# Performance work log

Hardware: AMD Instinct MI355X
Metric: run time of the kernel (lower is better)

## Reference

```python
import jax, jax.numpy as jnp
import numpy as np

B, F, T, D, O = 8192, 512, 64, 6, 128
N_INTERNAL = 2 ** D - 1  # 63
N_LEAVES = 2 ** D        # 64


def smooth_step(t):
    tc = jnp.clip(t, -0.5, 0.5)
    return -2.0 * tc ** 3 + 1.5 * tc + 0.5


def setup_inputs() -> dict:
    key = jax.random.key(0)
    k1, k2, k3, k4 = jax.random.split(key, 4)
    x = jax.random.normal(k1, (B, F), dtype=jnp.float32)
    # Stacked per-node Linear weights in BFS (heap) order: node i -> row i.
    W_nodes = jax.random.normal(k2, (N_INTERNAL, F, T), dtype=jnp.float32) * (1.0 / np.sqrt(F))
    b_nodes = jax.random.normal(k3, (N_INTERNAL, T), dtype=jnp.float32) * 0.01
    # Per-leaf mixing weight [out_features, num_trees], leaves in BFS order.
    W_leaf = jax.random.normal(k4, (N_LEAVES, O, T), dtype=jnp.float32)
    return {"x": x, "W_nodes": W_nodes, "b_nodes": b_nodes, "W_leaf": W_leaf}


def reference(x, W_nodes, b_nodes, W_leaf):
    n_internal = W_nodes.shape[0]
    depth = int(np.log2(n_internal + 1))
    # All internal-node gates in one stacked GEMM: [B, n_internal, T]
    s = smooth_step(jnp.einsum('bf,nft->bnt', x, W_nodes) + b_nodes[None, :, :])
    b, _, t = s.shape
    prob = jnp.ones((b, 1, t), dtype=s.dtype)  # root prob
    start = 0
    for lvl in range(depth):
        width = 2 ** lvl
        s_l = s[:, start:start + width]  # [B, width, T], nodes at this level
        start += width
        # node local j -> children local 2j (left, prob*s) and 2j+1 (right, prob*(1-s))
        prob = jnp.stack([prob * s_l, prob * (1.0 - s_l)], axis=2).reshape(b, 2 * width, t)
    # prob: [B, n_leaves, T]; mix per-leaf, per-tree weights -> [B, O]
    out = jnp.einsum('blt,lot->bo', prob, W_leaf)
    return out
```

## Files before the change

kernel.cpp:

```cpp
#include <hip/hip_runtime.h>
#include <hip/hip_fp16.h>

#define BATCH 8192
#define FDIM  512
#define NTREE 64
#define NODES 63
#define ODIM  128
#define NJP   4096
#define K2    4096
#define TPG   8

typedef _Float16 f16;
typedef _Float16 f16x2 __attribute__((ext_vector_type(2)));
typedef _Float16 f16x4 __attribute__((ext_vector_type(4)));
typedef _Float16 f16x8 __attribute__((ext_vector_type(8)));
typedef float    f32x4 __attribute__((ext_vector_type(4)));

#define XH_OFF   0
#define XH_SZ    ((size_t)BATCH*FDIM*2)
#define WNH_OFF  (XH_OFF + XH_SZ)
#define WNH_SZ   ((size_t)NJP*FDIM*2)
#define WLT_OFF  (WNH_OFF + WNH_SZ)
#define WLT_SZ   ((size_t)ODIM*K2*2)
#define WS_NEEDED (WLT_OFF + WLT_SZ)

__device__ __forceinline__ float smooth_step_f(float t) {
    float tc = fminf(fmaxf(t, -0.5f), 0.5f);
    return fmaf(tc, fmaf(-2.0f * tc, tc, 1.5f), 0.5f);
}

__device__ __forceinline__ int sw_off(int row, int g) {
    return ((row >> 3) * 512) + (((row & 7) * 8 + (g ^ (row & 7))) * 8);
}

__global__ __launch_bounds__(256)
void prep_kernel(const float* __restrict__ x, const float* __restrict__ wn,
                 const float* __restrict__ wl,
                 f16* __restrict__ xf, f16* __restrict__ wnf, f16* __restrict__ wlf,
                 float* __restrict__ out)
{
    const int bid = blockIdx.x, tid = threadIdx.x;
    if (bid >= 832) {
        size_t i = ((size_t)(bid - 832) * 256 + tid) * 4;
        f32x4 z = {};
        *(f32x4*)(out + i) = z;
        return;
    }
    if (bid < 512) {
        const int bx = bid >> 3, k0 = bid & 7;
        f16* dst = xf + ((size_t)bx * 8192 + (size_t)k0 * 1024) * 8;
        #pragma unroll
        for (int c = 0; c < 4; ++c) {
            int fid  = c * 256 + tid;
            int lane = fid & 63, ks = (fid >> 6) & 1, rg = (fid >> 7) & 7;
            int row  = bx * 128 + rg * 16 + (lane & 15);
            int k    = k0 * 64 + (ks * 4 + (lane >> 4)) * 8;
            const float* s = x + (size_t)row * FDIM + k;
            float4 a = *(const float4*)s, b = *(const float4*)(s + 4);
            f16x8 v = { (f16)a.x, (f16)a.y, (f16)a.z, (f16)a.w,
                        (f16)b.x, (f16)b.y, (f16)b.z, (f16)b.w };
            *(f16x8*)(dst + (size_t)fid * 8) = v;
        }
    } else if (bid < 768) {
        const int id = bid - 512;
        const int t0 = (id >> 4) * 4;
        const int n  = tid & 63;
        const int k8 = (id & 15) * 4 + (tid >> 6);
        float4 q[8];
        if (n != NODES) {
            #pragma unroll
            for (int e = 0; e < 8; ++e)
                q[e] = *(const float4*)(wn + ((size_t)n * FDIM + k8 * 8 + e) * NTREE + t0);
        }
        #pragma unroll
        for (int j = 0; j < 4; ++j) {
            int t  = t0 + j;
            int tp = t >> 1;
            int cg = (t & 1) * 4 + (n >> 4);
            size_t chunk = (size_t)tp * 8192 + (size_t)(k8 >> 3) * 1024 + cg * 128
                         + ((k8 >> 2) & 1) * 64 + (k8 & 3) * 16 + (n & 15);
            f16x8 v;
            if (n == NODES) {
                #pragma unroll
                for (int e = 0; e < 8; ++e) v[e] = (f16)0.0f;
            } else {
                const float* qf = (const float*)q;
                #pragma unroll
                for (int e = 0; e < 8; ++e) v[e] = (f16)qf[e * 4 + j];
            }
            *(f16x8*)(wnf + chunk * 8) = v;
        }
    } else {
        const int id = bid - 768;
        const int t0 = (id >> 2) * 4;
        const int o  = tid & 127;
        const int l8 = (id & 3) * 2 + (tid >> 7);
        float4 q[8];
        #pragma unroll
        for (int e = 0; e < 8; ++e)
            q[e] = *(const float4*)(wl + ((size_t)(l8 * 8 + e) * ODIM + o) * NTREE + t0);
        #pragma unroll
        for (int j = 0; j < 4; ++j) {
            int t  = t0 + j;
            int tp = t >> 1, h = t & 1;
            size_t chunk = (size_t)tp * 2048 + (size_t)h * 1024 + (o >> 4) * 128
                         + (l8 >> 2) * 64 + (l8 & 3) * 16 + (o & 15);
            const float* qf = (const float*)q;
            f16x8 v;
            #pragma unroll
            for (int e = 0; e < 8; ++e) v[e] = (f16)qf[e * 4 + j];
            *(f16x8*)(wlf + chunk * 8) = v;
        }
    }
}

__global__ __launch_bounds__(256, 2)
void fused_tree(const f16* __restrict__ xhF, const f16* __restrict__ wnhF,
                const float* __restrict__ bn, const f16* __restrict__ wltF,
                float* __restrict__ out)
{
    __shared__ __align__(16) f16 SH[16640];
    const int tid  = threadIdx.x;
    const int lane = tid & 63;
    const int w    = tid >> 6;
    const int wm   = w & 1;
    const int wq   = w >> 1;
    const int row0 = blockIdx.x * 128;
    const int tpg  = blockIdx.y;

    const int frow = tid & 127;
    const int ftr  = tid >> 7;

    const f16x8* __restrict__ xv = (const f16x8*)xhF;
    const f16x8* __restrict__ wv = (const f16x8*)wnhF;
    const f16x8* __restrict__ lv = (const f16x8*)wltF;
    const size_t xb = (size_t)blockIdx.x * 8192 + (size_t)wm * 512 + lane;

    f32x4 lacc[4][4] = {};

    for (int tpi = 0; tpi < 4; ++tpi) {
        const int tp = tpg * 4 + tpi;
        const int j0 = tp * 128;

        const size_t wb = (size_t)tp * 8192 + (size_t)wq * 512 + lane;
        f32x4 acc[4][4] = {};
        #pragma unroll 2
        for (int k0 = 0; k0 < 8; ++k0) {
            #pragma unroll
            for (int ks = 0; ks < 2; ++ks) {
                f16x8 bfr[4];
                #pragma unroll
                for (int tn = 0; tn < 4; ++tn)
                    bfr[tn] = wv[wb + k0 * 1024 + tn * 128 + ks * 64];
                #pragma unroll
                for (int tm = 0; tm < 4; ++tm) {
                    f16x8 afr = xv[xb + k0 * 1024 + tm * 128 + ks * 64];
                    #pragma unroll
                    for (int tn = 0; tn < 4; ++tn)
                        acc[tm][tn] = __builtin_amdgcn_mfma_f32_16x16x32_f16(afr, bfr[tn], acc[tm][tn], 0, 0, 0);
                }
            }
        }

        #pragma unroll
        for (int tn = 0; tn < 4; ++tn) {
            int col = wq * 64 + tn * 16 + (lane & 15);
            int nn  = col & 63;
            int tt  = (j0 + col) >> 6;
            float bias = (nn < NODES) ? bn[nn * NTREE + tt] : 0.0f;
            #pragma unroll
            for (int tm = 0; tm < 4; ++tm) {
                #pragma unroll
                for (int r = 0; r < 4; ++r) {
                    int row = wm * 64 + tm * 16 + (lane >> 4) * 4 + r;
                    SH[row * 130 + col] = (f16)smooth_step_f(acc[tm][tn][r] + bias);
                }
            }
        }
        __syncthreads();

        f16x8 ov[8];
        {
            const f16* gp = &SH[frow * 130 + ftr * 64];
            float gg[64];
            #pragma unroll
            for (int c = 0; c < 32; ++c) {
                f16x2 v = *(const f16x2*)(gp + 2 * c);
                gg[2 * c]     = (float)v[0];
                gg[2 * c + 1] = (float)v[1];
            }
            __syncthreads();
            float pr[32];
            pr[0] = 1.0f;
            int bse = 0;
            #pragma unroll
            for (int lvl = 0; lvl < 5; ++lvl) {
                const int width = 1 << lvl;
                #pragma unroll
                for (int i = width - 1; i >= 0; --i) {
                    float p = pr[i], s = gg[bse + i];
                    pr[2 * i]     = p * s;
                    pr[2 * i + 1] = p * (1.0f - s);
                }
                bse += width;
            }
            #pragma unroll
            for (int i = 0; i < 32; ++i) {
                float s5 = gg[31 + i];
                float p  = pr[i];
                ov[i >> 2][(i & 3) * 2]     = (f16)(p * s5);
                ov[i >> 2][(i & 3) * 2 + 1] = (f16)(p * (1.0f - s5));
            }
        }

        #pragma unroll
        for (int g2 = 0; g2 < 8; ++g2)
            *(f16x8*)&SH[ftr * 8192 + sw_off(frow, g2)] = ov[g2];
        __syncthreads();

        const size_t lb = (size_t)tp * 2048 + (size_t)wq * 512 + lane;
        #pragma unroll
        for (int h = 0; h < 2; ++h) {
            #pragma unroll
            for (int ks = 0; ks < 2; ++ks) {
                int g = ks * 4 + (lane >> 4);
                f16x8 bfr[4];
                #pragma unroll
                for (int tn = 0; tn < 4; ++tn)
                    bfr[tn] = lv[lb + h * 1024 + tn * 128 + ks * 64];
                #pragma unroll
                for (int tm = 0; tm < 4; ++tm) {
                    int m = wm * 64 + tm * 16 + (lane & 15);
                    f16x8 afr = *(const f16x8*)&SH[h * 8192 + sw_off(m, g)];
                    #pragma unroll
                    for (int tn = 0; tn < 4; ++tn)
                        lacc[tm][tn] = __builtin_amdgcn_mfma_f32_16x16x32_f16(afr, bfr[tn], lacc[tm][tn], 0, 0, 0);
                }
            }
        }
        __syncthreads();
    }

    #pragma unroll
    for (int tn = 0; tn < 4; ++tn) {
        int o = wq * 64 + tn * 16 + (lane & 15);
        #pragma unroll
        for (int tm = 0; tm < 4; ++tm) {
            #pragma unroll
            for (int r = 0; r < 4; ++r) {
                int row = row0 + wm * 64 + tm * 16 + (lane >> 4) * 4 + r;
                unsafeAtomicAdd(out + (size_t)row * ODIM + o, lacc[tm][tn][r]);
            }
        }
    }
}

#define ROWS 8
__global__ __launch_bounds__(256, 2)
void soft_tree_fallback(const float* __restrict__ x, const float* __restrict__ Wn,
                        const float* __restrict__ bn, const float* __restrict__ Wl,
                        float* __restrict__ out)
{
    __shared__ __half s_lds[ROWS][NODES][NTREE];
    const int lane = threadIdx.x & 63;
    const int w    = threadIdx.x >> 6;
    const long row0 = (long)blockIdx.x * ROWS;
    for (int n = w; n < NODES; n += 4) {
        const float* wp = Wn + ((long)n * FDIM) * NTREE + lane;
        const float* xp = x + row0 * FDIM;
        float acc[ROWS];
        #pragma unroll
        for (int r = 0; r < ROWS; ++r) acc[r] = 0.0f;
        #pragma unroll 8
        for (int f = 0; f < FDIM; ++f) {
            float wv = wp[(long)f * NTREE];
            #pragma unroll
            for (int r = 0; r < ROWS; ++r)
                acc[r] = fmaf(xp[r * FDIM + f], wv, acc[r]);
        }
        float bias = bn[n * NTREE + lane];
        #pragma unroll
        for (int r = 0; r < ROWS; ++r)
            s_lds[r][n][lane] = __float2half(smooth_step_f(acc[r] + bias));
    }
    __syncthreads();
    const int r0 = w * 2, r1 = w * 2 + 1;
    float pr0[64], pr1[64];
    {
        pr0[0] = 1.0f; pr1[0] = 1.0f;
        int base = 0;
        #pragma unroll
        for (int lvl = 0; lvl < 6; ++lvl) {
            const int width = 1 << lvl;
            #pragma unroll
            for (int i = width - 1; i >= 0; --i) {
                float sa = __half2float(s_lds[r0][base + i][lane]);
                float sb = __half2float(s_lds[r1][base + i][lane]);
                float pa = pr0[i], pb = pr1[i];
                pr0[2 * i] = pa * sa; pr0[2 * i + 1] = pa * (1.0f - sa);
                pr1[2 * i] = pb * sb; pr1[2 * i + 1] = pb * (1.0f - sb);
            }
            base += width;
        }
    }
    for (int o = 0; o < ODIM; ++o) {
        const float* wlp = Wl + (long)o * NTREE + lane;
        float c0 = 0.0f, c1 = 0.0f;
        #pragma unroll
        for (int l = 0; l < 64; ++l) {
            float wv = wlp[(long)l * (ODIM * NTREE)];
            c0 = fmaf(pr0[l], wv, c0);
            c1 = fmaf(pr1[l], wv, c1);
        }
        #pragma unroll
        for (int off = 32; off > 0; off >>= 1) {
            c0 += __shfl_xor(c0, off, 64);
            c1 += __shfl_xor(c1, off, 64);
        }
        if (lane == 0) {
            out[(row0 + r0) * ODIM + o] = c0;
            out[(row0 + r1) * ODIM + o] = c1;
        }
    }
}

extern "C" void kernel_launch(void* const* d_in, const int* in_sizes, int n_in,
                              void* d_out, int out_size, void* d_ws, size_t ws_size,
                              hipStream_t stream) {
    const float* x  = (const float*)d_in[0];
    const float* Wn = (const float*)d_in[1];
    const float* bn = (const float*)d_in[2];
    const float* Wl = (const float*)d_in[3];
    float* out = (float*)d_out;

    if (ws_size < WS_NEEDED) {
        soft_tree_fallback<<<BATCH / ROWS, 256, 0, stream>>>(x, Wn, bn, Wl, out);
        return;
    }

    f16* xh  = (f16*)((char*)d_ws + XH_OFF);
    f16* wnh = (f16*)((char*)d_ws + WNH_OFF);
    f16* wlt = (f16*)((char*)d_ws + WLT_OFF);

    prep_kernel<<<832 + 1024, 256, 0, stream>>>(x, Wn, Wl, xh, wnh, wlt, out);
    fused_tree<<<dim3(BATCH / 128, TPG), 256, 0, stream>>>(xh, wnh, bn, wlt, out);
}
```

Baseline: 159.8 us.

## Split tree-pair groups finer and replace atomic output with partial-sum reduction

Doubles the grid's tree-group dimension so each block handles two tree pairs instead of four, and raises the occupancy hint to four blocks per CU. Blocks now write their leaf-mix results to per-group partial buffers instead of atomically adding into the output, and a new reduce kernel sums the 16 partials. The output zeroing in the prep kernel is removed. This aims for more parallelism and no atomic contention, at the cost of 64 MB of partial writes and reads plus a third kernel launch.

```diff
diff --git a/kernel.cpp b/kernel.cpp
--- a/kernel.cpp
+++ b/kernel.cpp
@@ -8,7 +8,7 @@
 #define ODIM  128
 #define NJP   4096
 #define K2    4096
-#define TPG   8
+#define TPG   16
 
 typedef _Float16 f16;
 typedef _Float16 f16x2 __attribute__((ext_vector_type(2)));
@@ -22,7 +22,9 @@
 #define WNH_SZ   ((size_t)NJP*FDIM*2)
 #define WLT_OFF  (WNH_OFF + WNH_SZ)
 #define WLT_SZ   ((size_t)ODIM*K2*2)
-#define WS_NEEDED (WLT_OFF + WLT_SZ)
+#define PS_OFF   (WLT_OFF + WLT_SZ)
+#define PS_SZ    ((size_t)TPG*BATCH*ODIM*4)
+#define WS_NEEDED (PS_OFF + PS_SZ)
 
 __device__ __forceinline__ float smooth_step_f(float t) {
     float tc = fminf(fmaxf(t, -0.5f), 0.5f);
@@ -36,16 +38,9 @@
 __global__ __launch_bounds__(256)
 void prep_kernel(const float* __restrict__ x, const float* __restrict__ wn,
                  const float* __restrict__ wl,
-                 f16* __restrict__ xf, f16* __restrict__ wnf, f16* __restrict__ wlf,
-                 float* __restrict__ out)
+                 f16* __restrict__ xf, f16* __restrict__ wnf, f16* __restrict__ wlf)
 {
     const int bid = blockIdx.x, tid = threadIdx.x;
-    if (bid >= 832) {
-        size_t i = ((size_t)(bid - 832) * 256 + tid) * 4;
-        f32x4 z = {};
-        *(f32x4*)(out + i) = z;
-        return;
-    }
     if (bid < 512) {
         const int bx = bid >> 3, k0 = bid & 7;
         f16* dst = xf + ((size_t)bx * 8192 + (size_t)k0 * 1024) * 8;
@@ -114,10 +109,10 @@
     }
 }
 
-__global__ __launch_bounds__(256, 2)
+__global__ __launch_bounds__(256, 4)
 void fused_tree(const f16* __restrict__ xhF, const f16* __restrict__ wnhF,
                 const float* __restrict__ bn, const f16* __restrict__ wltF,
-                float* __restrict__ out)
+                float* __restrict__ partial)
 {
     __shared__ __align__(16) f16 SH[16640];
     const int tid  = threadIdx.x;
@@ -138,8 +133,8 @@
 
     f32x4 lacc[4][4] = {};
 
-    for (int tpi = 0; tpi < 4; ++tpi) {
-        const int tp = tpg * 4 + tpi;
+    for (int tpi = 0; tpi < 2; ++tpi) {
+        const int tp = tpg * 2 + tpi;
         const int j0 = tp * 128;
 
         const size_t wb = (size_t)tp * 8192 + (size_t)wq * 512 + lane;
@@ -241,6 +236,7 @@
         __syncthreads();
     }
 
+    float* dst = partial + (size_t)tpg * BATCH * ODIM;
     #pragma unroll
     for (int tn = 0; tn < 4; ++tn) {
         int o = wq * 64 + tn * 16 + (lane & 15);
@@ -249,10 +245,19 @@
             #pragma unroll
             for (int r = 0; r < 4; ++r) {
                 int row = row0 + wm * 64 + tm * 16 + (lane >> 4) * 4 + r;
-                unsafeAtomicAdd(out + (size_t)row * ODIM + o, lacc[tm][tn][r]);
-            }
-        }
-    }
+                dst[(size_t)row * ODIM + o] = lacc[tm][tn][r];
+            }
+        }
+    }
+}
+
+__global__ void reduce_kernel(const float* __restrict__ partial, float* __restrict__ out) {
+    size_t i = ((size_t)blockIdx.x * blockDim.x + threadIdx.x) * 4;
+    f32x4 a = *(const f32x4*)(partial + i);
+    #pragma unroll
+    for (int k = 1; k < TPG; ++k)
+        a += *(const f32x4*)(partial + (size_t)k * BATCH * ODIM + i);
+    *(f32x4*)(out + i) = a;
 }
 
 #define ROWS 8
@@ -338,10 +343,12 @@
         return;
     }
 
-    f16* xh  = (f16*)((char*)d_ws + XH_OFF);
-    f16* wnh = (f16*)((char*)d_ws + WNH_OFF);
-    f16* wlt = (f16*)((char*)d_ws + WLT_OFF);
-
-    prep_kernel<<<832 + 1024, 256, 0, stream>>>(x, Wn, Wl, xh, wnh, wlt, out);
-    fused_tree<<<dim3(BATCH / 128, TPG), 256, 0, stream>>>(xh, wnh, bn, wlt, out);
-}
+    f16*   xh  = (f16*)((char*)d_ws + XH_OFF);
+    f16*   wnh = (f16*)((char*)d_ws + WNH_OFF);
+    f16*   wlt = (f16*)((char*)d_ws + WLT_OFF);
+    float* ps  = (float*)((char*)d_ws + PS_OFF);
+
+    prep_kernel<<<832, 256, 0, stream>>>(x, Wn, Wl, xh, wnh, wlt);
+    fused_tree<<<dim3(BATCH / 128, TPG), 256, 0, stream>>>(xh, wnh, bn, wlt, ps);
+    reduce_kernel<<<(BATCH * ODIM) / (256 * 4), 256, 0, stream>>>(ps, out);
+}
```

After: 193.5 us. 21.0% more time.
